# Performance work log

Hardware: AMD Instinct MI355X
Metric: run time of the kernel (lower is better)

Reference implementation:

```python
import jax, jax.numpy as jnp
import numpy as np

N_NODES = 100000
N_EDGES = 1600000
N_CRYS = 2000
NODE_F = 64
EDGE_F = 41
N_CONV = 3
H_F = 128
EPS = 1e-5


def _seg_mean(v, idx, n):
    s = jax.ops.segment_sum(v, idx, num_segments=n)
    c = jax.ops.segment_sum(jnp.ones((v.shape[0], 1), v.dtype), idx, num_segments=n)
    return s / jnp.maximum(c, 1.0)


def _bn(x, g, b):
    # training-mode batch norm over dim 0, biased variance (torch semantics)
    m = x.mean(axis=0)
    v = x.var(axis=0)
    return (x - m) * jax.lax.rsqrt(v + EPS) * g + b


def setup_inputs() -> dict:
    key = jax.random.key(0)
    ks = jax.random.split(key, 16)
    inp = {}
    inp['node_fea'] = jax.random.randint(ks[0], (N_NODES,), 0, 101)
    inp['edge_fea'] = jax.random.normal(ks[1], (N_EDGES, EDGE_F), dtype=jnp.float32)
    inp['idx1'] = jax.random.randint(ks[2], (N_EDGES,), 0, N_NODES)
    inp['idx2'] = jax.random.randint(ks[3], (N_EDGES,), 0, N_NODES)
    inp['idx3'] = jnp.sort(jax.random.randint(ks[4], (N_NODES,), 0, N_CRYS))
    # parameters
    din = 2 * NODE_F + EDGE_F
    sc = 1.0 / np.sqrt(din)
    inp['emb'] = jax.random.normal(ks[5], (101, NODE_F), dtype=jnp.float32)
    inp['Wf'] = jax.random.uniform(ks[6], (N_CONV, din, 2 * NODE_F), jnp.float32, -sc, sc)
    inp['bf'] = jax.random.uniform(ks[7], (N_CONV, 2 * NODE_F), jnp.float32, -sc, sc)
    inp['g1'] = jnp.ones((N_CONV, 2 * NODE_F), jnp.float32)
    inp['be1'] = jnp.zeros((N_CONV, 2 * NODE_F), jnp.float32)
    inp['g2'] = jnp.ones((N_CONV, NODE_F), jnp.float32)
    inp['be2'] = jnp.zeros((N_CONV, NODE_F), jnp.float32)
    sc2 = 1.0 / np.sqrt(NODE_F)
    inp['Wc'] = jax.random.uniform(ks[8], (NODE_F, H_F), jnp.float32, -sc2, sc2)
    inp['bc'] = jax.random.uniform(ks[9], (H_F,), jnp.float32, -sc2, sc2)
    sc3 = 1.0 / np.sqrt(H_F)
    inp['Wo'] = jax.random.uniform(ks[10], (H_F, 2), jnp.float32, -sc3, sc3)
    inp['bo'] = jax.random.uniform(ks[11], (2,), jnp.float32, -sc3, sc3)
    return inp


def reference(node_fea, edge_fea, idx1, idx2, idx3, emb, Wf, bf, g1, be1, g2, be2, Wc, bc, Wo, bo):
    x = emb[node_fea]                                   # [N, 64]
    for l in range(N_CONV):
        z12 = jnp.concatenate([x[idx1], x[idx2], edge_fea], axis=1)   # [E, 169]
        z12 = _bn(z12 @ Wf[l] + bf[l], g1[l], be1[l])   # [E, 128]
        gate, conv = jnp.split(z12, 2, axis=1)
        msg = jax.nn.sigmoid(gate) * jax.nn.softplus(conv)
        node_new = _bn(_seg_mean(msg, idx1, N_NODES), g2[l], be2[l])
        x = jax.nn.softplus(x + node_new)
    crys = _seg_mean(x, idx3, N_CRYS)                   # [C, 64]
    crys = jax.nn.softplus(crys @ Wc + bc)              # [C, 128]
    return crys @ Wo + bo                               # [C, 2]
```

## Files before the change

### kernel.cpp

```cpp
#include <hip/hip_runtime.h>
#include <hip/hip_bf16.h>


#define NN 100000
#define NE 1600000
#define NC 2000
#define KPAD 176
#define EFW 48
#define EPSB 1e-5f
#define NCH 1000
#define CH 100

typedef _Float16 f16;
typedef _Float16 half8 __attribute__((ext_vector_type(8)));
typedef _Float16 half2v __attribute__((ext_vector_type(2)));
typedef float f32x16 __attribute__((ext_vector_type(16)));

__device__ __forceinline__ f32x16 zero16() {
    f32x16 v;
#pragma unroll
    for (int i = 0; i < 16; i++) v[i] = 0.f;
    return v;
}
__device__ __forceinline__ float fsoftplus(float x) {
    return fmaxf(x, 0.f) + __logf(1.f + __expf(-fabsf(x)));
}
__device__ __forceinline__ float fsigmoid(float x) {
    return __fdividef(1.f, 1.f + __expf(-x));
}

__global__ void k_prep_x(const int* __restrict__ nf, const float* __restrict__ emb,
                         float* __restrict__ xf, f16* __restrict__ x16) {
    for (int idx = blockIdx.x * blockDim.x + threadIdx.x; idx < NN * 64;
         idx += gridDim.x * blockDim.x) {
        int n = idx >> 6, k = idx & 63;
        float v = emb[nf[n] * 64 + k];
        xf[idx] = v;
        x16[idx] = (f16)v;
    }
}

__global__ void k_deg(const int* __restrict__ idx1, const int* __restrict__ idx3,
                      int* deg1, float* cnt3) {
    for (int i = blockIdx.x * blockDim.x + threadIdx.x; i < NE;
         i += gridDim.x * blockDim.x) {
        atomicAdd(&deg1[idx1[i]], 1);
        if (i < NN) atomicAdd(&cnt3[idx3[i]], 1.f);
    }
}

__global__ void k_scan_a(const int* __restrict__ deg, int* __restrict__ csum) {
    int t = blockIdx.x * blockDim.x + threadIdx.x;
    if (t < NCH) {
        int s = 0;
        int base = t * CH;
        for (int i = 0; i < CH; i++) s += deg[base + i];
        csum[t] = s;
    }
}
__global__ void k_scan_b(const int* __restrict__ csum, int* __restrict__ coff) {
    __shared__ int sc[256];
    int t = threadIdx.x;
    int v[4];
    int part = 0;
#pragma unroll
    for (int q = 0; q < 4; q++) {
        int idx = 4 * t + q;
        v[q] = (idx < NCH) ? csum[idx] : 0;
        part += v[q];
    }
    sc[t] = part;
    __syncthreads();
    for (int off = 1; off < 256; off <<= 1) {
        int add = (t >= off) ? sc[t - off] : 0;
        __syncthreads();
        sc[t] += add;
        __syncthreads();
    }
    int run = sc[t] - part;
#pragma unroll
    for (int q = 0; q < 4; q++) {
        int idx = 4 * t + q;
        if (idx < NCH) coff[idx] = run;
        run += v[q];
    }
}
__global__ void k_scan_c(const int* __restrict__ deg, const int* __restrict__ coff,
                         int* __restrict__ rp) {
    int t = blockIdx.x * blockDim.x + threadIdx.x;
    if (t < NCH) {
        int running = coff[t];
        int base = t * CH;
        for (int i = 0; i < CH; i++) {
            rp[base + i] = running;
            running += deg[base + i];
        }
    }
}

__global__ void k_scatter(const int* __restrict__ idx1, const int* __restrict__ idx2,
                          const int* __restrict__ rp1, int* cur1, int* elist1,
                          int* i1r, int* i2r) {
    for (int e = blockIdx.x * blockDim.x + threadIdx.x; e < NE;
         e += gridDim.x * blockDim.x) {
        int n1 = idx1[e];
        int p = rp1[n1] + atomicAdd(&cur1[n1], 1);
        elist1[p] = e;
        i1r[p] = n1;
        i2r[p] = idx2[e];
    }
}

__global__ void k_prep_efg(const float* __restrict__ ef, const int* __restrict__ elist1,
                           f16* __restrict__ ef16p) {
    for (long idx = (long)blockIdx.x * blockDim.x + threadIdx.x; idx < (long)NE * EFW;
         idx += (long)gridDim.x * blockDim.x) {
        long p = idx / EFW;
        int k = (int)(idx - p * EFW);
        int e = elist1[p];
        float v = (k < 41) ? ef[(size_t)e * 41 + k] : 0.f;
        ef16p[idx] = (f16)v;
    }
}

__global__ void k_wt(const float* __restrict__ Wf_l, f16* __restrict__ WT) {
    for (int idx = blockIdx.x * blockDim.x + threadIdx.x; idx < 128 * KPAD;
         idx += gridDim.x * blockDim.x) {
        int col = idx / KPAD, k = idx % KPAD;
        float v = (k < 169) ? Wf_l[k * 128 + col] : 0.f;
        WT[idx] = (f16)v;
    }
}

__global__ __launch_bounds__(256) void k_edge_a(
    const f16* __restrict__ x16, const f16* __restrict__ ef16p,
    const f16* __restrict__ WT, const int* __restrict__ i1r,
    const int* __restrict__ i2r, float* __restrict__ estats,
    half2v* __restrict__ zp) {
    __shared__ float lst[256];
    int tid = threadIdx.x;
    int lane = tid & 63;
    int w = tid >> 6;
    int h = w >> 1, ch = w & 1;
    int c = lane & 31, kg = lane >> 5;

    half8 bfr[2][11];
#pragma unroll
    for (int t = 0; t < 2; t++) {
        int col = 32 * ch + 64 * t + c;
        const f16* bp = WT + col * KPAD + kg * 8;
#pragma unroll
        for (int s = 0; s < 11; s++)
            bfr[t][s] = *reinterpret_cast<const half8*>(bp + s * 16);
    }

    lst[tid] = 0.f;
    __syncthreads();

    float s1[2] = {0.f, 0.f}, s2[2] = {0.f, 0.f};
    const int NT = NE / 64;
    for (int tile = blockIdx.x; tile < NT; tile += gridDim.x) {
        int p0 = tile * 64 + h * 32;
        long p = p0 + c;
        int i1 = i1r[p], i2 = i2r[p];
        f32x16 acc0 = zero16(), acc1 = zero16();
#pragma unroll
        for (int s = 0; s < 4; s++) {
            half8 a = *reinterpret_cast<const half8*>(x16 + (size_t)i1 * 64 + s * 16 + kg * 8);
            acc0 = __builtin_amdgcn_mfma_f32_32x32x16_f16(a, bfr[0][s], acc0, 0, 0, 0);
            acc1 = __builtin_amdgcn_mfma_f32_32x32x16_f16(a, bfr[1][s], acc1, 0, 0, 0);
        }
#pragma unroll
        for (int s = 0; s < 4; s++) {
            half8 a = *reinterpret_cast<const half8*>(x16 + (size_t)i2 * 64 + s * 16 + kg * 8);
            acc0 = __builtin_amdgcn_mfma_f32_32x32x16_f16(a, bfr[0][4 + s], acc0, 0, 0, 0);
            acc1 = __builtin_amdgcn_mfma_f32_32x32x16_f16(a, bfr[1][4 + s], acc1, 0, 0, 0);
        }
#pragma unroll
        for (int s = 0; s < 3; s++) {
            half8 a = *reinterpret_cast<const half8*>(ef16p + p * EFW + s * 16 + kg * 8);
            acc0 = __builtin_amdgcn_mfma_f32_32x32x16_f16(a, bfr[0][8 + s], acc0, 0, 0, 0);
            acc1 = __builtin_amdgcn_mfma_f32_32x32x16_f16(a, bfr[1][8 + s], acc1, 0, 0, 0);
        }
#pragma unroll
        for (int r = 0; r < 16; r++) {
            float v0 = acc0[r], v1 = acc1[r];
            s1[0] += v0; s2[0] += v0 * v0;
            s1[1] += v1; s2[1] += v1 * v1;
            int row = (r & 3) + 8 * (r >> 2) + 4 * kg;
            half2v pr;
            pr[0] = (f16)v0;
            pr[1] = (f16)v1;
            zp[(size_t)(p0 + row) * 64 + 32 * ch + c] = pr;
        }
    }
#pragma unroll
    for (int t = 0; t < 2; t++) {
        s1[t] += __shfl_xor(s1[t], 32, 64);
        s2[t] += __shfl_xor(s2[t], 32, 64);
    }
    if (kg == 0) {
#pragma unroll
        for (int t = 0; t < 2; t++) {
            int col = 32 * ch + 64 * t + c;
            atomicAdd(&lst[col], s1[t]);
            atomicAdd(&lst[128 + col], s2[t]);
        }
    }
    __syncthreads();
    atomicAdd(&estats[tid], lst[tid]);
}

__global__ __launch_bounds__(256) void k_nodered(
    const half2v* __restrict__ zp, const int* __restrict__ rp1,
    const int* __restrict__ deg1, const float* __restrict__ estats,
    const float* __restrict__ g1, const float* __restrict__ be1,
    float* __restrict__ raw_out, float* __restrict__ nstats) {
    __shared__ float sstat[128];
    int tid = threadIdx.x;
    int j = tid & 63, wv = tid >> 6;
    if (tid < 128) sstat[tid] = 0.f;
    __syncthreads();
    float mg = estats[j] * (1.f / NE);
    float vg = estats[128 + j] * (1.f / NE) - mg * mg;
    float ag = g1[j] * rsqrtf(vg + EPSB);
    float bg = be1[j] - mg * ag;
    float mc = estats[64 + j] * (1.f / NE);
    float vc = estats[192 + j] * (1.f / NE) - mc * mc;
    float ac = g1[64 + j] * rsqrtf(vc + EPSB);
    float bc = be1[64 + j] - mc * ac;
    float p1 = 0.f, p2 = 0.f;
    for (int n = blockIdx.x * 4 + wv; n < NN; n += gridDim.x * 4) {
        int st = rp1[n], d = deg1[n];
        float acc = 0.f;
        for (int q = 0; q < d; q++) {
            half2v z = zp[(size_t)(st + q) * 64 + j];
            float g = fsigmoid((float)z[0] * ag + bg);
            float s = fsoftplus((float)z[1] * ac + bc);
            acc += g * s;
        }
        float raw = acc / fmaxf((float)d, 1.f);
        raw_out[(size_t)n * 64 + j] = raw;
        p1 += raw;
        p2 += raw * raw;
    }
    atomicAdd(&sstat[j], p1);
    atomicAdd(&sstat[64 + j], p2);
    __syncthreads();
    if (tid < 128) atomicAdd(&nstats[tid], sstat[tid]);
}

template <bool LAST>
__global__ __launch_bounds__(256) void k_node_apply(
    const float* __restrict__ raw_in, const float* __restrict__ nstats,
    const float* __restrict__ g2, const float* __restrict__ be2,
    float* __restrict__ xf, f16* __restrict__ x16, const int* __restrict__ idx3,
    float* __restrict__ crsum) {
    for (int idx = blockIdx.x * blockDim.x + threadIdx.x; idx < NN * 64;
         idx += gridDim.x * blockDim.x) {
        int n = idx >> 6, j = idx & 63;
        float m = nstats[j] * (1.f / NN);
        float var = nstats[64 + j] * (1.f / NN) - m * m;
        float rs = rsqrtf(var + EPSB);
        float a = g2[j] * rs;
        float b = be2[j] - m * a;
        float v = fsoftplus(xf[idx] + raw_in[idx] * a + b);
        if (LAST) {
            atomicAdd(&crsum[(size_t)idx3[n] * 64 + j], v);
        } else {
            xf[idx] = v;
            x16[idx] = (f16)v;
        }
    }
}

__global__ __launch_bounds__(128) void k_out(const float* __restrict__ crsum,
                                             const float* __restrict__ cnt3,
                                             const float* __restrict__ Wc,
                                             const float* __restrict__ bcv,
                                             const float* __restrict__ Wo,
                                             const float* __restrict__ bo,
                                             float* __restrict__ out) {
    __shared__ float crym[64];
    __shared__ float red[4];
    int c = blockIdx.x, tid = threadIdx.x;
    if (tid < 64) crym[tid] = crsum[c * 64 + tid] / fmaxf(cnt3[c], 1.f);
    __syncthreads();
    float hv = bcv[tid];
#pragma unroll
    for (int k = 0; k < 64; k++) hv += crym[k] * Wc[k * 128 + tid];
    hv = fsoftplus(hv);
    float o0 = hv * Wo[tid * 2 + 0];
    float o1 = hv * Wo[tid * 2 + 1];
#pragma unroll
    for (int off = 32; off > 0; off >>= 1) {
        o0 += __shfl_down(o0, off, 64);
        o1 += __shfl_down(o1, off, 64);
    }
    int wv = tid >> 6;
    if ((tid & 63) == 0) { red[wv * 2] = o0; red[wv * 2 + 1] = o1; }
    __syncthreads();
    if (tid == 0) {
        out[c * 2 + 0] = red[0] + red[2] + bo[0];
        out[c * 2 + 1] = red[1] + red[3] + bo[1];
    }
}

static inline size_t al256(size_t x) { return (x + 255) & ~(size_t)255; }

extern "C" void kernel_launch(void* const* d_in, const int* in_sizes, int n_in,
                              void* d_out, int out_size, void* d_ws, size_t ws_size,
                              hipStream_t stream) {
    const int* node_fea = (const int*)d_in[0];
    const float* edge_fea = (const float*)d_in[1];
    const int* idx1 = (const int*)d_in[2];
    const int* idx2 = (const int*)d_in[3];
    const int* idx3 = (const int*)d_in[4];
    const float* emb = (const float*)d_in[5];
    const float* Wf = (const float*)d_in[6];
    const float* g1 = (const float*)d_in[8];
    const float* be1 = (const float*)d_in[9];
    const float* g2 = (const float*)d_in[10];
    const float* be2 = (const float*)d_in[11];
    const float* Wc = (const float*)d_in[12];
    const float* bc = (const float*)d_in[13];
    const float* Wo = (const float*)d_in[14];
    const float* bo = (const float*)d_in[15];
    float* out = (float*)d_out;
    unsigned char* ws = (unsigned char*)d_ws;

    size_t off = 0;
    size_t o_xf = off;     off = al256(off + (size_t)NN * 64 * 4);
    size_t o_x16 = off;    off = al256(off + (size_t)NN * 64 * 2);
    size_t o_efp = off;    off = al256(off + (size_t)NE * EFW * 2);
    size_t o_WT = off;     off = al256(off + (size_t)128 * KPAD * 2);
    size_t o_rp1 = off;    off = al256(off + (size_t)NN * 4);
    size_t o_el1 = off;    off = al256(off + (size_t)NE * 4);
    size_t o_i1r = off;    off = al256(off + (size_t)NE * 4);
    size_t o_i2r = off;    off = al256(off + (size_t)NE * 4);
    size_t o_raw = off;    off = al256(off + (size_t)NN * 64 * 4);
    size_t o_deg1 = off;   off = al256(off + (size_t)NN * 4);
    size_t o_cur1 = off;   off = al256(off + (size_t)NN * 4);
    size_t o_cnt3 = off;   off = al256(off + (size_t)NC * 4);
    size_t o_csum = off;   off = al256(off + 1024 * 4);
    size_t o_coff = off;   off = al256(off + 1024 * 4);
    size_t o_crsum = off;  off = al256(off + (size_t)NC * 64 * 4);
    size_t prep_zero_end = off;
    size_t o_estats = off; off = al256(off + 256 * 4);
    size_t o_nstats = off; off = al256(off + 128 * 4);
    size_t layer_zero_end = off;
    size_t o_z = off;      off = al256(off + (size_t)NE * 64 * 4);
    (void)ws_size;

    float* xf = (float*)(ws + o_xf);
    f16* x16 = (f16*)(ws + o_x16);
    f16* ef16p = (f16*)(ws + o_efp);
    f16* WT = (f16*)(ws + o_WT);
    int* rp1 = (int*)(ws + o_rp1);
    int* elist1 = (int*)(ws + o_el1);
    int* i1r = (int*)(ws + o_i1r);
    int* i2r = (int*)(ws + o_i2r);
    float* raw = (float*)(ws + o_raw);
    int* deg1 = (int*)(ws + o_deg1);
    int* cur1 = (int*)(ws + o_cur1);
    float* cnt3 = (float*)(ws + o_cnt3);
    int* csum = (int*)(ws + o_csum);
    int* coff = (int*)(ws + o_coff);
    float* crsum = (float*)(ws + o_crsum);
    float* estats = (float*)(ws + o_estats);
    float* nstats = (float*)(ws + o_nstats);
    half2v* zp = (half2v*)(ws + o_z);

    hipMemsetAsync(ws + o_deg1, 0, prep_zero_end - o_deg1, stream);
    k_prep_x<<<1024, 256, 0, stream>>>(node_fea, emb, xf, x16);
    k_deg<<<2048, 256, 0, stream>>>(idx1, idx3, deg1, cnt3);
    k_scan_a<<<4, 256, 0, stream>>>(deg1, csum);
    k_scan_b<<<1, 256, 0, stream>>>(csum, coff);
    k_scan_c<<<4, 256, 0, stream>>>(deg1, coff, rp1);
    k_scatter<<<2048, 256, 0, stream>>>(idx1, idx2, rp1, cur1, elist1, i1r, i2r);
    k_prep_efg<<<4096, 256, 0, stream>>>(edge_fea, elist1, ef16p);

    for (int l = 0; l < 3; l++) {
        const float* Wf_l = Wf + (size_t)l * 169 * 128;
        hipMemsetAsync(ws + o_estats, 0, layer_zero_end - o_estats, stream);
        k_wt<<<88, 256, 0, stream>>>(Wf_l, WT);
        k_edge_a<<<2048, 256, 0, stream>>>(x16, ef16p, WT, i1r, i2r, estats, zp);
        k_nodered<<<4096, 256, 0, stream>>>(zp, rp1, deg1, estats, g1 + l * 128,
                                            be1 + l * 128, raw, nstats);
        if (l < 2) {
            k_node_apply<false><<<1024, 256, 0, stream>>>(raw, nstats, g2 + l * 64,
                                                          be2 + l * 64, xf, x16,
                                                          idx3, crsum);
        } else {
            k_node_apply<true><<<1024, 256, 0, stream>>>(raw, nstats, g2 + l * 64,
                                                         be2 + l * 64, xf, x16,
                                                         idx3, crsum);
        }
    }
    k_out<<<2000, 128, 0, stream>>>(crsum, cnt3, Wc, bc, Wo, bo, out);
}
```

Baseline: 1.911 ms.

## Split edge GEMM across four waves per 32-edge tile with scalar fp16 stores

The edge kernel now processes one 32-edge tile per block, with each of the four waves computing 32 output columns, instead of two 32-edge halves each split over two column groups. Each wave holds one accumulator and half the weight fragments, which lowers register pressure and may raise occupancy. The cost is that every gathered x row is loaded by all four waves, and outputs are written as individual nontemporal fp16 stores in the same interleaved layout. The node-reduce loop is unrolled with nontemporal loads, and the edge grid is doubled.

```diff
diff --git a/kernel.cpp b/kernel.cpp
--- a/kernel.cpp
+++ b/kernel.cpp
@@ -136,76 +136,59 @@
     const f16* __restrict__ x16, const f16* __restrict__ ef16p,
     const f16* __restrict__ WT, const int* __restrict__ i1r,
     const int* __restrict__ i2r, float* __restrict__ estats,
-    half2v* __restrict__ zp) {
+    f16* __restrict__ zph) {
     __shared__ float lst[256];
     int tid = threadIdx.x;
     int lane = tid & 63;
-    int w = tid >> 6;
-    int h = w >> 1, ch = w & 1;
+    int q = tid >> 6;
     int c = lane & 31, kg = lane >> 5;
-
-    half8 bfr[2][11];
-#pragma unroll
-    for (int t = 0; t < 2; t++) {
-        int col = 32 * ch + 64 * t + c;
+    int col = 32 * q + c;
+
+    half8 bfr[11];
+    {
         const f16* bp = WT + col * KPAD + kg * 8;
 #pragma unroll
         for (int s = 0; s < 11; s++)
-            bfr[t][s] = *reinterpret_cast<const half8*>(bp + s * 16);
-    }
-
-    lst[tid] = 0.f;
-    __syncthreads();
-
-    float s1[2] = {0.f, 0.f}, s2[2] = {0.f, 0.f};
-    const int NT = NE / 64;
+            bfr[s] = *reinterpret_cast<const half8*>(bp + s * 16);
+    }
+    const size_t zoff = 2 * (size_t)(col & 63) + (col >> 6);
+
+    float s1 = 0.f, s2 = 0.f;
+    const int NT = NE / 32;
     for (int tile = blockIdx.x; tile < NT; tile += gridDim.x) {
-        int p0 = tile * 64 + h * 32;
+        int p0 = tile * 32;
         long p = p0 + c;
         int i1 = i1r[p], i2 = i2r[p];
-        f32x16 acc0 = zero16(), acc1 = zero16();
+        f32x16 acc = zero16();
 #pragma unroll
         for (int s = 0; s < 4; s++) {
             half8 a = *reinterpret_cast<const half8*>(x16 + (size_t)i1 * 64 + s * 16 + kg * 8);
-            acc0 = __builtin_amdgcn_mfma_f32_32x32x16_f16(a, bfr[0][s], acc0, 0, 0, 0);
-            acc1 = __builtin_amdgcn_mfma_f32_32x32x16_f16(a, bfr[1][s], acc1, 0, 0, 0);
+            acc = __builtin_amdgcn_mfma_f32_32x32x16_f16(a, bfr[s], acc, 0, 0, 0);
         }
 #pragma unroll
         for (int s = 0; s < 4; s++) {
             half8 a = *reinterpret_cast<const half8*>(x16 + (size_t)i2 * 64 + s * 16 + kg * 8);
-            acc0 = __builtin_amdgcn_mfma_f32_32x32x16_f16(a, bfr[0][4 + s], acc0, 0, 0, 0);
-            acc1 = __builtin_amdgcn_mfma_f32_32x32x16_f16(a, bfr[1][4 + s], acc1, 0, 0, 0);
+            acc = __builtin_amdgcn_mfma_f32_32x32x16_f16(a, bfr[4 + s], acc, 0, 0, 0);
         }
 #pragma unroll
         for (int s = 0; s < 3; s++) {
             half8 a = *reinterpret_cast<const half8*>(ef16p + p * EFW + s * 16 + kg * 8);
-            acc0 = __builtin_amdgcn_mfma_f32_32x32x16_f16(a, bfr[0][8 + s], acc0, 0, 0, 0);
-            acc1 = __builtin_amdgcn_mfma_f32_32x32x16_f16(a, bfr[1][8 + s], acc1, 0, 0, 0);
+            acc = __builtin_amdgcn_mfma_f32_32x32x16_f16(a, bfr[8 + s], acc, 0, 0, 0);
         }
 #pragma unroll
         for (int r = 0; r < 16; r++) {
-            float v0 = acc0[r], v1 = acc1[r];
-            s1[0] += v0; s2[0] += v0 * v0;
-            s1[1] += v1; s2[1] += v1 * v1;
+            float v = acc[r];
+            s1 += v;
+            s2 += v * v;
             int row = (r & 3) + 8 * (r >> 2) + 4 * kg;
-            half2v pr;
-            pr[0] = (f16)v0;
-            pr[1] = (f16)v1;
-            zp[(size_t)(p0 + row) * 64 + 32 * ch + c] = pr;
-        }
-    }
-#pragma unroll
-    for (int t = 0; t < 2; t++) {
-        s1[t] += __shfl_xor(s1[t], 32, 64);
-        s2[t] += __shfl_xor(s2[t], 32, 64);
-    }
+            __builtin_nontemporal_store((f16)v, &zph[(size_t)(p0 + row) * 128 + zoff]);
+        }
+    }
+    s1 += __shfl_xor(s1, 32, 64);
+    s2 += __shfl_xor(s2, 32, 64);
     if (kg == 0) {
-#pragma unroll
-        for (int t = 0; t < 2; t++) {
-            int col = 32 * ch + 64 * t + c;
-            atomicAdd(&lst[col], s1[t]);
-            atomicAdd(&lst[128 + col], s2[t]);
-        }
+        lst[col] = s1;
+        lst[128 + col] = s2;
     }
     __syncthreads();
     atomicAdd(&estats[tid], lst[tid]);
@@ -233,8 +216,9 @@
     for (int n = blockIdx.x * 4 + wv; n < NN; n += gridDim.x * 4) {
         int st = rp1[n], d = deg1[n];
         float acc = 0.f;
+#pragma unroll 4
         for (int q = 0; q < d; q++) {
-            half2v z = zp[(size_t)(st + q) * 64 + j];
+            half2v z = __builtin_nontemporal_load(&zp[(size_t)(st + q) * 64 + j]);
             float g = fsigmoid((float)z[0] * ag + bg);
             float s = fsoftplus((float)z[1] * ac + bc);
             acc += g * s;
@@ -369,6 +353,7 @@
     float* crsum = (float*)(ws + o_crsum);
     float* estats = (float*)(ws + o_estats);
     float* nstats = (float*)(ws + o_nstats);
+    f16* zph = (f16*)(ws + o_z);
     half2v* zp = (half2v*)(ws + o_z);
 
     hipMemsetAsync(ws + o_deg1, 0, prep_zero_end - o_deg1, stream);
@@ -384,7 +369,7 @@
         const float* Wf_l = Wf + (size_t)l * 169 * 128;
         hipMemsetAsync(ws + o_estats, 0, layer_zero_end - o_estats, stream);
         k_wt<<<88, 256, 0, stream>>>(Wf_l, WT);
-        k_edge_a<<<2048, 256, 0, stream>>>(x16, ef16p, WT, i1r, i2r, estats, zp);
+        k_edge_a<<<4096, 256, 0, stream>>>(x16, ef16p, WT, i1r, i2r, estats, zph);
         k_nodered<<<4096, 256, 0, stream>>>(zp, rp1, deg1, estats, g1 + l * 128,
                                             be1 + l * 128, raw, nstats);
         if (l < 2) {
```

New measurement: 1.820 ms. -4.8%, faster.
